# Optimization experiments

Measured on AMD Instinct MI355X. Metric: run time of the kernel, lower is better.

Reference implementation:

```python
import jax, jax.numpy as jnp
import numpy as np

B, H, W, C = 4, 64, 64, 256
CD = C // 8

def setup_inputs() -> dict:
    key = jax.random.key(0)
    ks = jax.random.split(key, 4)
    x = jax.random.normal(ks[0], (B, H, W, C), dtype=jnp.float32)
    Wf = jax.random.normal(ks[1], (C, CD), dtype=jnp.float32) * (1.0 / np.sqrt(C))
    Wg = jax.random.normal(ks[2], (C, CD), dtype=jnp.float32) * (1.0 / np.sqrt(C))
    Wh = jax.random.normal(ks[3], (C, C), dtype=jnp.float32) * (1.0 / np.sqrt(C))
    bf = jnp.zeros((CD,), dtype=jnp.float32)
    bg = jnp.zeros((CD,), dtype=jnp.float32)
    bh = jnp.zeros((C,), dtype=jnp.float32)
    return {"x": x, "Wf": Wf, "bf": bf, "Wg": Wg, "bg": bg, "Wh": Wh, "bh": bh}

def reference(x, Wf, bf, Wg, bg, Wh, bh):
    b, h, w, c = x.shape
    n = h * w
    xf = x.reshape(b, n, c)                       # [B,N,C]
    f = xf @ Wf + bf                              # [B,N,C/8] (1x1 conv == per-token linear)
    g = xf @ Wg + bg                              # [B,N,C/8]
    hh = xf @ Wh + bh                             # [B,N,C]
    s = jnp.einsum('bnd,bmd->bnm', g, f)          # g @ f^T, unscaled
    attn = jax.nn.softmax(s, axis=-1)             # [B,N,N]
    o = jnp.einsum('bnm,bmc->bnc', attn, hh)      # [B,N,C]
    return x + o.reshape(b, h, w, c)
```

## Files before the change

### kernel.cpp

```cpp
#include <hip/hip_runtime.h>
#include <hip/hip_bf16.h>
#include <stdint.h>

#define NN 4096
#define CC 256
#define DD 32
#define QP 20
#define CHW 17408

typedef short    bf16x8 __attribute__((ext_vector_type(8)));
typedef _Float16 f16x8  __attribute__((ext_vector_type(8)));
typedef float    f32x4  __attribute__((ext_vector_type(4)));

__device__ __forceinline__ unsigned short bf16_rne(float x) {
    union { float f; unsigned int u; } v; v.f = x;
    unsigned int u = v.u;
    return (unsigned short)((u + 0x7FFFu + ((u >> 16) & 1u)) >> 16);
}
__device__ __forceinline__ float bf16f(unsigned short h) {
    union { float f; unsigned int u; } v; v.u = ((unsigned int)h) << 16; return v.f;
}
__device__ __forceinline__ unsigned short f16_bits(float x) {
    union { _Float16 h; unsigned short u; } v; v.h = (_Float16)x;
    return v.u;
}
__device__ __forceinline__ void load_lds16(const unsigned short* g, unsigned short* l) {
    __builtin_amdgcn_global_load_lds(
        (const __attribute__((address_space(1))) unsigned int*)g,
        (__attribute__((address_space(3))) unsigned int*)l, 16, 0, 0);
}

__global__ __launch_bounds__(256) void prep_kernel(
    const float* __restrict__ Wf, const float* __restrict__ Wg,
    const float* __restrict__ Wh, unsigned short* __restrict__ Wst)
{
    int id  = blockIdx.x * 256 + threadIdx.x;
    int ks  = id / 12288;
    int rem = id - ks * 12288;
    int row = rem >> 5;
    int k   = ks * 32 + (rem & 31);
    unsigned short outv;
    if (row < 256) {
        outv = bf16_rne(Wh[(size_t)k * CC + row]);
    } else if (row < 320) {
        int d = row - 256;
        float v = (d < 32) ? Wf[(size_t)k * DD + d] : Wg[(size_t)k * DD + (d - 32)];
        outv = bf16_rne(v);
    } else {
        int d = row - 320;
        float v = (d < 32) ? Wf[(size_t)k * DD + d] : Wg[(size_t)k * DD + (d - 32)];
        unsigned short h = bf16_rne(v);
        outv = bf16_rne(v - bf16f(h));
    }
    Wst[id] = outv;
}

__global__ __launch_bounds__(256, 2) void proj_kernel(
    const float* __restrict__ x,
    const float* __restrict__ bfv, const float* __restrict__ bgv,
    const float* __restrict__ bhv,
    const unsigned short* __restrict__ Wst,
    unsigned short* __restrict__ f16b, unsigned short* __restrict__ g16b,
    unsigned short* __restrict__ hhT)
{
    const int tid  = threadIdx.x;
    const int lane = tid & 63;
    const int wv   = tid >> 6;
    const int col  = lane & 15;
    const int quad = lane >> 4;
    const int tok0 = blockIdx.x * 32;
    const int b    = tok0 >> 12;

    __shared__ __align__(16) unsigned short xh[32 * 272];
    __shared__ __align__(16) unsigned short xl[32 * 272];
    __shared__ __align__(16) unsigned short WT[1920 * 8];

    #pragma unroll
    for (int it = 0; it < 8; ++it) {
        int idx = it * 1024 + tid * 4;
        float4 v = *(const float4*)(x + (size_t)tok0 * CC + idx);
        int tok = idx >> 8, k = idx & 255;
        unsigned short h0 = bf16_rne(v.x), h1 = bf16_rne(v.y),
                       h2 = bf16_rne(v.z), h3 = bf16_rne(v.w);
        uint2 wh_, wl_;
        wh_.x = (unsigned int)h0 | ((unsigned int)h1 << 16);
        wh_.y = (unsigned int)h2 | ((unsigned int)h3 << 16);
        wl_.x = (unsigned int)bf16_rne(v.x - bf16f(h0)) |
                ((unsigned int)bf16_rne(v.y - bf16f(h1)) << 16);
        wl_.y = (unsigned int)bf16_rne(v.z - bf16f(h2)) |
                ((unsigned int)bf16_rne(v.w - bf16f(h3)) << 16);
        *(uint2*)&xh[tok * 272 + k] = wh_;
        *(uint2*)&xl[tok * 272 + k] = wl_;
    }

    f32x4 acc[5][2];
    #pragma unroll
    for (int t = 0; t < 5; ++t) {
        int tl = wv * 5 + t;
        float bias;
        if (tl < 16) bias = bhv[tl * 16 + col];
        else { int fd = (tl - 16) * 16 + col;
               bias = (fd < 32) ? bfv[fd] : bgv[fd - 32]; }
        acc[t][0] = (f32x4){bias, bias, bias, bias};
        acc[t][1] = (f32x4){bias, bias, bias, bias};
    }

    for (int ks = 0; ks < 8; ++ks) {
        for (int t = 0; t < 8; ++t) {
            int i = wv + t * 4;
            if (i >= 30) break;
            int l = i * 64 + lane;
            int row = l / 5, g = l - row * 5;
            const unsigned short* gp = (g < 4)
                ? (Wst + (size_t)ks * 12288 + row * 32 + g * 8)
                : (Wst + (size_t)ks * 12288);
            load_lds16(gp, &WT[i * 512]);
        }
        __syncthreads();

        bf16x8 ah[2], al[2];
        #pragma unroll
        for (int mt = 0; mt < 2; ++mt) {
            ah[mt] = *(const bf16x8*)&xh[(mt * 16 + col) * 272 + ks * 32 + quad * 8];
            al[mt] = *(const bf16x8*)&xl[(mt * 16 + col) * 272 + ks * 32 + quad * 8];
        }

        #pragma unroll
        for (int t = 0; t < 5; ++t) {
            int tl = wv * 5 + t;
            int wrow = (tl < 16) ? (tl * 16 + col) : (256 + (tl - 16) * 16 + col);
            bf16x8 bh = *(const bf16x8*)&WT[wrow * 40 + quad * 8];
            #pragma unroll
            for (int mt = 0; mt < 2; ++mt) {
                acc[t][mt] = __builtin_amdgcn_mfma_f32_16x16x32_bf16(ah[mt], bh, acc[t][mt], 0, 0, 0);
                acc[t][mt] = __builtin_amdgcn_mfma_f32_16x16x32_bf16(al[mt], bh, acc[t][mt], 0, 0, 0);
            }
            if (tl >= 16) {
                bf16x8 bl = *(const bf16x8*)&WT[(wrow + 64) * 40 + quad * 8];
                #pragma unroll
                for (int mt = 0; mt < 2; ++mt)
                    acc[t][mt] = __builtin_amdgcn_mfma_f32_16x16x32_bf16(ah[mt], bl, acc[t][mt], 0, 0, 0);
            }
        }
        __syncthreads();
    }

    const int ks_h = (tok0 & 63) >> 5;
    const int kc   = (tok0 & 4095) >> 6;
    const size_t tbase = ((size_t)(b * 64 + kc)) * CHW;
    #pragma unroll
    for (int t = 0; t < 5; ++t) {
        int tl = wv * 5 + t;
        if (tl < 16) {
            #pragma unroll
            for (int mt = 0; mt < 2; ++mt) {
                int qk = mt * 2 + (quad >> 1);
                int jb = (quad & 1) * 4;
                uint2 w;
                w.x = (unsigned int)bf16_rne(acc[t][mt][0]) | ((unsigned int)bf16_rne(acc[t][mt][1]) << 16);
                w.y = (unsigned int)bf16_rne(acc[t][mt][2]) | ((unsigned int)bf16_rne(acc[t][mt][3]) << 16);
                *(uint2*)&hhT[tbase + (size_t)(((ks_h * 17 + tl) * 64) + qk * 16 + col) * 8 + jb] = w;
            }
        } else {
            int fd = (tl - 16) * 16 + col;
            unsigned short* dst = (fd < 32) ? f16b : g16b;
            int d = fd & 31;
            #pragma unroll
            for (int mt = 0; mt < 2; ++mt)
                #pragma unroll
                for (int r = 0; r < 4; ++r) {
                    int tok = tok0 + mt * 16 + quad * 4 + r;
                    dst[(size_t)tok * DD + d] = f16_bits(acc[t][mt][r]);
                }
        }
    }
    #pragma unroll
    for (int it = 0; it < 2; ++it) {
        int e = tid + it * 256;
        int j = e & 7, ck = (e >> 3) & 15, qk = e >> 7;
        hhT[tbase + (size_t)(((ks_h * 17 + 16) * 64) + qk * 16 + ck) * 8 + j] =
            (ck == 0) ? (unsigned short)0x3F80 : (unsigned short)0;
    }
}

__global__ __launch_bounds__(256, 2) void attn_kernel(
    const unsigned short* __restrict__ g16b,
    const unsigned short* __restrict__ f16b,
    const unsigned short* __restrict__ hhT,
    float* __restrict__ O0,
    float* __restrict__ O1,
    float* __restrict__ lbuf)
{
    const int tid  = threadIdx.x;
    const int lane = tid & 63;
    const int wv   = tid >> 6;
    const int col  = lane & 15;
    const int quad = lane >> 4;
    const int bid  = blockIdx.x;
    const int sp   = bid & 1;
    const int b    = (bid >> 1) & 3;
    const int qblk = bid >> 3;
    const int q0   = qblk * 64 + wv * 16;
    const int kcb  = sp * 32;

    __shared__ __align__(16) unsigned short hbuf[2][CHW];
    __shared__ __align__(8)  unsigned short p_all[4][64 * QP];
    unsigned short* p_lds = p_all[wv];

    const unsigned short* fb16 = f16b + (size_t)b * NN * DD;
    const unsigned short* hb   = hhT + (size_t)b * 64 * CHW;

    const f16x8 a_g = *(const f16x8*)(g16b + ((size_t)(b * NN + q0 + col)) * DD + quad * 8);

    f32x4 zero = {0.f, 0.f, 0.f, 0.f};
    f32x4 acc[17];
    #pragma unroll
    for (int i = 0; i < 17; ++i) acc[i] = zero;

    {
        const unsigned short* tile = hb + (size_t)kcb * CHW;
        for (int t = 0; t < 9; ++t) {
            int i = wv + t * 4;
            if (i >= 34) break;
            load_lds16(tile + (size_t)(i * 64 + lane) * 8, &hbuf[0][i * 512]);
        }
    }
    __syncthreads();

    for (int kc = 0; kc < 32; ++kc) {
        const int nb  = kc & 1;
        const int kk0 = (kcb + kc) * 64;

        if (kc + 1 < 32) {
            const unsigned short* tile = hb + (size_t)(kcb + kc + 1) * CHW;
            for (int t = 0; t < 9; ++t) {
                int i = wv + t * 4;
                if (i >= 34) break;
                load_lds16(tile + (size_t)(i * 64 + lane) * 8, &hbuf[nb ^ 1][i * 512]);
            }
        }

        f32x4 s_t[4];
        #pragma unroll
        for (int kt = 0; kt < 4; ++kt) {
            f16x8 bf_ = *(const f16x8*)(fb16 + (size_t)(kk0 + kt * 16 + col) * DD + quad * 8);
            s_t[kt] = __builtin_amdgcn_mfma_f32_16x16x32_f16(a_g, bf_, zero, 0, 0, 0);
        }

        #pragma unroll
        for (int kt = 0; kt < 4; ++kt) {
            unsigned short pv[4];
            #pragma unroll
            for (int r = 0; r < 4; ++r)
                pv[r] = bf16_rne(__expf(s_t[kt][r] - 40.0f));
            uint2 w2;
            w2.x = (unsigned int)pv[0] | ((unsigned int)pv[1] << 16);
            w2.y = (unsigned int)pv[2] | ((unsigned int)pv[3] << 16);
            *(uint2*)&p_lds[(kt * 16 + col) * QP + quad * 4] = w2;
        }

        bf16x8 a_p[2];
        #pragma unroll
        for (int ks = 0; ks < 2; ++ks)
            #pragma unroll
            for (int j = 0; j < 8; ++j)
                a_p[ks][j] = (short)p_lds[(ks * 32 + quad * 8 + j) * QP + col];

        #pragma unroll
        for (int ks = 0; ks < 2; ++ks) {
            bf16x8 bh[17];
            #pragma unroll
            for (int ct = 0; ct < 17; ++ct)
                bh[ct] = *(const bf16x8*)&hbuf[nb][(size_t)(((ks * 17 + ct) * 64) + lane) * 8];
            #pragma unroll
            for (int ct = 0; ct < 17; ++ct)
                acc[ct] = __builtin_amdgcn_mfma_f32_16x16x32_bf16(a_p[ks], bh[ct], acc[ct], 0, 0, 0);
        }

        __syncthreads();
    }

    float* Op = sp ? O1 : O0;
    const size_t obase = (size_t)(b * NN + q0) * CC;
    #pragma unroll
    for (int ct = 0; ct < 16; ++ct) {
        #pragma unroll
        for (int r = 0; r < 4; ++r)
            Op[obase + (size_t)(quad * 4 + r) * CC + ct * 16 + col] = acc[ct][r];
    }
    if (col == 0) {
        #pragma unroll
        for (int r = 0; r < 4; ++r)
            lbuf[sp * (4 * NN) + b * NN + q0 + quad * 4 + r] = acc[16][r];
    }
}

__global__ __launch_bounds__(256) void reduce_kernel(
    const float* __restrict__ x, const float* __restrict__ O1,
    const float* __restrict__ lbuf, float* __restrict__ out)
{
    int id = blockIdx.x * 256 + threadIdx.x;
    int q  = id >> 6;
    int c4 = (id & 63) * 4;
    size_t base = (size_t)q * CC + c4;
    float inv = 1.0f / (lbuf[q] + lbuf[4 * NN + q]);
    float4 o0 = *(const float4*)(out + base);
    float4 o1 = *(const float4*)(O1 + base);
    float4 xv = *(const float4*)(x + base);
    float4 r;
    r.x = xv.x + (o0.x + o1.x) * inv;
    r.y = xv.y + (o0.y + o1.y) * inv;
    r.z = xv.z + (o0.z + o1.z) * inv;
    r.w = xv.w + (o0.w + o1.w) * inv;
    *(float4*)(out + base) = r;
}

extern "C" void kernel_launch(void* const* d_in, const int* in_sizes, int n_in,
                              void* d_out, int out_size, void* d_ws, size_t ws_size,
                              hipStream_t stream) {
    const float* x  = (const float*)d_in[0];
    const float* Wf = (const float*)d_in[1];
    const float* bf = (const float*)d_in[2];
    const float* Wg = (const float*)d_in[3];
    const float* bg = (const float*)d_in[4];
    const float* Wh = (const float*)d_in[5];
    const float* bh = (const float*)d_in[6];
    float* out = (float*)d_out;

    unsigned char* ws = (unsigned char*)d_ws;
    unsigned short* Wst  = (unsigned short*)(ws);
    unsigned short* f16b = (unsigned short*)(ws + 0x040000);
    unsigned short* g16b = (unsigned short*)(ws + 0x140000);
    unsigned short* hhT  = (unsigned short*)(ws + 0x240000);
    float*          O1   = (float*)(ws + 0xAC0000);
    float*          lbuf = (float*)(ws + 0x1AC0000);

    prep_kernel<<<384, 256, 0, stream>>>(Wf, Wg, Wh, Wst);
    proj_kernel<<<512, 256, 0, stream>>>(x, bf, bg, bh, Wst, f16b, g16b, hhT);
    attn_kernel<<<512, 256, 0, stream>>>(g16b, f16b, hhT, out, O1, lbuf);
    reduce_kernel<<<4096, 256, 0, stream>>>(x, O1, lbuf, out);
}
```

Baseline: 163.1 us.

## Give each attention wave 32 query rows to reuse LDS value fragments

The attention kernel now runs 2 waves per block instead of 4, and each wave handles 32 query rows as two 16-row tiles. Every value fragment read from LDS then feeds two MFMAs, which halves LDS read traffic per FLOP. The key loop is split into two 32-key halves so the P tile stays small, and the P staging buffer is re-laid out with padding 36. The cost is twice the accumulator registers (34 f32x4), fewer waves per block, and launch bounds of (128,1), all of which may reduce occupancy and latency hiding.

```diff
diff --git a/kernel.cpp b/kernel.cpp
--- a/kernel.cpp
+++ b/kernel.cpp
@@ -5,7 +5,7 @@
 #define NN 4096
 #define CC 256
 #define DD 32
-#define QP 20
+#define PP 36
 #define CHW 17408
 
 typedef short    bf16x8 __attribute__((ext_vector_type(8)));
@@ -183,7 +183,7 @@
     }
 }
 
-__global__ __launch_bounds__(256, 2) void attn_kernel(
+__global__ __launch_bounds__(128, 1) void attn_kernel(
     const unsigned short* __restrict__ g16b,
     const unsigned short* __restrict__ f16b,
     const unsigned short* __restrict__ hhT,
@@ -200,28 +200,33 @@
     const int sp   = bid & 1;
     const int b    = (bid >> 1) & 3;
     const int qblk = bid >> 3;
-    const int q0   = qblk * 64 + wv * 16;
+    const int q0   = qblk * 64 + wv * 32;
     const int kcb  = sp * 32;
 
     __shared__ __align__(16) unsigned short hbuf[2][CHW];
-    __shared__ __align__(8)  unsigned short p_all[4][64 * QP];
+    __shared__ __align__(8)  unsigned short p_all[2][32 * PP];
     unsigned short* p_lds = p_all[wv];
 
     const unsigned short* fb16 = f16b + (size_t)b * NN * DD;
     const unsigned short* hb   = hhT + (size_t)b * 64 * CHW;
 
-    const f16x8 a_g = *(const f16x8*)(g16b + ((size_t)(b * NN + q0 + col)) * DD + quad * 8);
+    f16x8 a_g[2];
+    #pragma unroll
+    for (int a = 0; a < 2; ++a)
+        a_g[a] = *(const f16x8*)(g16b + ((size_t)(b * NN + q0 + a * 16 + col)) * DD + quad * 8);
 
     f32x4 zero = {0.f, 0.f, 0.f, 0.f};
-    f32x4 acc[17];
-    #pragma unroll
-    for (int i = 0; i < 17; ++i) acc[i] = zero;
+    f32x4 acc[2][17];
+    #pragma unroll
+    for (int a = 0; a < 2; ++a)
+        #pragma unroll
+        for (int i = 0; i < 17; ++i) acc[a][i] = zero;
 
     {
         const unsigned short* tile = hb + (size_t)kcb * CHW;
-        for (int t = 0; t < 9; ++t) {
-            int i = wv + t * 4;
-            if (i >= 34) break;
+        #pragma unroll
+        for (int t = 0; t < 17; ++t) {
+            int i = wv + t * 2;
             load_lds16(tile + (size_t)(i * 64 + lane) * 8, &hbuf[0][i * 512]);
         }
     }
@@ -233,65 +238,72 @@
 
         if (kc + 1 < 32) {
             const unsigned short* tile = hb + (size_t)(kcb + kc + 1) * CHW;
-            for (int t = 0; t < 9; ++t) {
-                int i = wv + t * 4;
-                if (i >= 34) break;
+            #pragma unroll
+            for (int t = 0; t < 17; ++t) {
+                int i = wv + t * 2;
                 load_lds16(tile + (size_t)(i * 64 + lane) * 8, &hbuf[nb ^ 1][i * 512]);
             }
         }
 
-        f32x4 s_t[4];
-        #pragma unroll
-        for (int kt = 0; kt < 4; ++kt) {
-            f16x8 bf_ = *(const f16x8*)(fb16 + (size_t)(kk0 + kt * 16 + col) * DD + quad * 8);
-            s_t[kt] = __builtin_amdgcn_mfma_f32_16x16x32_f16(a_g, bf_, zero, 0, 0, 0);
-        }
-
-        #pragma unroll
-        for (int kt = 0; kt < 4; ++kt) {
-            unsigned short pv[4];
+        #pragma unroll
+        for (int half = 0; half < 2; ++half) {
+            f32x4 s_t[2][2];
+            #pragma unroll
+            for (int ktl = 0; ktl < 2; ++ktl) {
+                f16x8 bf_ = *(const f16x8*)(fb16 +
+                    (size_t)(kk0 + half * 32 + ktl * 16 + col) * DD + quad * 8);
+                #pragma unroll
+                for (int a = 0; a < 2; ++a)
+                    s_t[ktl][a] = __builtin_amdgcn_mfma_f32_16x16x32_f16(a_g[a], bf_, zero, 0, 0, 0);
+            }
+
+            #pragma unroll
+            for (int ktl = 0; ktl < 2; ++ktl)
+                #pragma unroll
+                for (int a = 0; a < 2; ++a) {
+                    unsigned short pv[4];
+                    #pragma unroll
+                    for (int r = 0; r < 4; ++r)
+                        pv[r] = bf16_rne(__expf(s_t[ktl][a][r] - 40.0f));
+                    uint2 w2;
+                    w2.x = (unsigned int)pv[0] | ((unsigned int)pv[1] << 16);
+                    w2.y = (unsigned int)pv[2] | ((unsigned int)pv[3] << 16);
+                    *(uint2*)&p_lds[(ktl * 16 + col) * PP + a * 16 + quad * 4] = w2;
+                }
+
+            bf16x8 a_p[2];
+            #pragma unroll
+            for (int a = 0; a < 2; ++a)
+                #pragma unroll
+                for (int j = 0; j < 8; ++j)
+                    a_p[a][j] = (short)p_lds[(quad * 8 + j) * PP + a * 16 + col];
+
+            #pragma unroll
+            for (int ct = 0; ct < 17; ++ct) {
+                bf16x8 bh = *(const bf16x8*)&hbuf[nb][(size_t)(((half * 17 + ct) * 64) + lane) * 8];
+                acc[0][ct] = __builtin_amdgcn_mfma_f32_16x16x32_bf16(a_p[0], bh, acc[0][ct], 0, 0, 0);
+                acc[1][ct] = __builtin_amdgcn_mfma_f32_16x16x32_bf16(a_p[1], bh, acc[1][ct], 0, 0, 0);
+            }
+        }
+
+        __syncthreads();
+    }
+
+    float* Op = sp ? O1 : O0;
+    #pragma unroll
+    for (int a = 0; a < 2; ++a) {
+        const size_t obase = (size_t)(b * NN + q0 + a * 16) * CC;
+        #pragma unroll
+        for (int ct = 0; ct < 16; ++ct) {
             #pragma unroll
             for (int r = 0; r < 4; ++r)
-                pv[r] = bf16_rne(__expf(s_t[kt][r] - 40.0f));
-            uint2 w2;
-            w2.x = (unsigned int)pv[0] | ((unsigned int)pv[1] << 16);
-            w2.y = (unsigned int)pv[2] | ((unsigned int)pv[3] << 16);
-            *(uint2*)&p_lds[(kt * 16 + col) * QP + quad * 4] = w2;
-        }
-
-        bf16x8 a_p[2];
-        #pragma unroll
-        for (int ks = 0; ks < 2; ++ks)
-            #pragma unroll
-            for (int j = 0; j < 8; ++j)
-                a_p[ks][j] = (short)p_lds[(ks * 32 + quad * 8 + j) * QP + col];
-
-        #pragma unroll
-        for (int ks = 0; ks < 2; ++ks) {
-            bf16x8 bh[17];
-            #pragma unroll
-            for (int ct = 0; ct < 17; ++ct)
-                bh[ct] = *(const bf16x8*)&hbuf[nb][(size_t)(((ks * 17 + ct) * 64) + lane) * 8];
-            #pragma unroll
-            for (int ct = 0; ct < 17; ++ct)
-                acc[ct] = __builtin_amdgcn_mfma_f32_16x16x32_bf16(a_p[ks], bh[ct], acc[ct], 0, 0, 0);
-        }
-
-        __syncthreads();
-    }
-
-    float* Op = sp ? O1 : O0;
-    const size_t obase = (size_t)(b * NN + q0) * CC;
-    #pragma unroll
-    for (int ct = 0; ct < 16; ++ct) {
-        #pragma unroll
-        for (int r = 0; r < 4; ++r)
-            Op[obase + (size_t)(quad * 4 + r) * CC + ct * 16 + col] = acc[ct][r];
-    }
-    if (col == 0) {
-        #pragma unroll
-        for (int r = 0; r < 4; ++r)
-            lbuf[sp * (4 * NN) + b * NN + q0 + quad * 4 + r] = acc[16][r];
+                Op[obase + (size_t)(quad * 4 + r) * CC + ct * 16 + col] = acc[a][ct][r];
+        }
+        if (col == 0) {
+            #pragma unroll
+            for (int r = 0; r < 4; ++r)
+                lbuf[sp * (4 * NN) + b * NN + q0 + a * 16 + quad * 4 + r] = acc[a][16][r];
+        }
     }
 }
 
@@ -337,6 +349,6 @@
 
     prep_kernel<<<384, 256, 0, stream>>>(Wf, Wg, Wh, Wst);
     proj_kernel<<<512, 256, 0, stream>>>(x, bf, bg, bh, Wst, f16b, g16b, hhT);
-    attn_kernel<<<512, 256, 0, stream>>>(g16b, f16b, hhT, out, O1, lbuf);
+    attn_kernel<<<512, 128, 0, stream>>>(g16b, f16b, hhT, out, O1, lbuf);
     reduce_kernel<<<4096, 256, 0, stream>>>(x, O1, lbuf, out);
 }
```

Result: slower. 198.4 us (+21.7%).
